# Kernel tuning notes

Hardware: AMD Instinct MI355X
Metric: run time of the kernel (lower is better)

The kernel has to match this reference:

```python
import jax, jax.numpy as jnp
import numpy as np

B, N, C, H = 32, 129, 768, 12
HID = 4 * C
EPS = 1e-5
NEG = -65504.0


def _layer_norm(x, g, b):
    mu = jnp.mean(x, axis=-1, keepdims=True)
    var = jnp.mean((x - mu) ** 2, axis=-1, keepdims=True)
    return (x - mu) / jnp.sqrt(var + EPS) * g + b


def _attn(x, m, g, b, wqkv, wproj):
    # x: [B, Nn, C], m: [B, Nn, 1] binary float mask
    Bb, Nn, Cc = x.shape
    hd = Cc // H
    xm = _layer_norm(x, g, b) * m
    qkv = (xm @ wqkv).reshape(Bb, Nn, 3, H, hd)
    q, k, v = (jnp.swapaxes(qkv[:, :, i], 1, 2) for i in range(3))  # [B,H,Nn,hd]
    att = jnp.einsum('bhqd,bhkd->bhqk', q, k) * (hd ** -0.5)
    outer = (m @ jnp.swapaxes(m, -1, -2))[:, None]  # [B,1,Nn,Nn] mask outer product
    att = jnp.where(outer == 0.0, NEG, att)
    att = jax.nn.softmax(att, axis=-1) * m[:, None]  # zero masked query rows
    out = jnp.einsum('bhqk,bhkd->bhqd', att, v)
    out = jnp.swapaxes(out, 1, 2).reshape(Bb, Nn, Cc)
    return out @ wproj


def _mlp(x, m, g, b, w1, w2):
    xm = _layer_norm(x, g, b) * m
    return jax.nn.gelu(xm @ w1, approximate=False) @ w2


def setup_inputs() -> dict:
    key = jax.random.key(0)
    ks = jax.random.split(key, 10)
    std = 0.02
    return {
        'RGB': jax.random.normal(ks[0], (B, N, C), jnp.float32),
        'NIR': jax.random.normal(ks[1], (B, N, C), jnp.float32),
        'TIR': jax.random.normal(ks[2], (B, N, C), jnp.float32),
        'mask': (jax.random.uniform(ks[3], (B, N - 1, 1)) > 0.3).astype(jnp.float32),
        'label': jax.random.randint(ks[4], (B,), 0, 171),
        # stacked params for branches [R, N, T, concat]
        'ln_g1': jnp.ones((4, C), jnp.float32),
        'ln_b1': jnp.zeros((4, C), jnp.float32),
        'w_qkv': std * jax.random.normal(ks[5], (4, C, 3 * C), jnp.float32),
        'w_proj': std * jax.random.normal(ks[6], (4, C, C), jnp.float32),
        'ln_g2': jnp.ones((4, C), jnp.float32),
        'ln_b2': jnp.zeros((4, C), jnp.float32),
        'w_fc1': std * jax.random.normal(ks[7], (4, C, HID), jnp.float32),
        'w_fc2': std * jax.random.normal(ks[8], (4, HID, C), jnp.float32),
        'out_g': jnp.ones((C,), jnp.float32),
        'out_b': jnp.zeros((C,), jnp.float32),
    }


def reference(RGB, NIR, TIR, mask, label, ln_g1, ln_b1, w_qkv, w_proj,
              ln_g2, ln_b2, w_fc1, w_fc2, out_g, out_b):
    m = jnp.concatenate([jnp.ones((RGB.shape[0], 1, 1), RGB.dtype), mask], axis=1)  # [B,N,1]

    def branch(x, i, mm):
        x = x + _attn(x, mm, ln_g1[i], ln_b1[i], w_qkv[i], w_proj[i])
        x = x + _mlp(x, mm, ln_g2[i], ln_b2[i], w_fc1[i], w_fc2[i])
        return x

    RGB = branch(RGB, 0, m)
    NIR = branch(NIR, 1, m)
    TIR = branch(TIR, 2, m)
    x = jnp.concatenate([RGB, NIR, TIR], axis=1)  # [B, 3N, C]
    m3 = jnp.tile(m, (1, 3, 1))
    x = branch(x, 3, m3)
    x = _layer_norm(x, out_g, out_b) * m3
    return x
```

## Files before the change

### kernel.cpp

```cpp
#include <hip/hip_runtime.h>

typedef unsigned short u16;
typedef __attribute__((ext_vector_type(4))) float f32x4;
typedef __attribute__((ext_vector_type(8))) short s16x8;
typedef __attribute__((ext_vector_type(4))) short s16x4;
typedef __attribute__((ext_vector_type(4))) unsigned short u16x4;

#define HH 12
#define CC 768
#define AS1(p) ((const __attribute__((address_space(1))) void*)(p))
#define AS3(p) ((__attribute__((address_space(3))) void*)(p))

__device__ inline u16 f2bf(float x){
  unsigned u = __float_as_uint(x);
  u = (u + 0x7FFFu + ((u >> 16) & 1u)) >> 16;
  return (u16)u;
}

__device__ inline f32x4 mfma32(s16x8 a, s16x8 b, f32x4 c){
  return __builtin_amdgcn_mfma_f32_16x16x32_bf16(a, b, c, 0, 0, 0);
}
__device__ inline f32x4 mfma16(s16x4 a, s16x4 b, f32x4 c){
  return __builtin_amdgcn_mfma_f32_16x16x16bf16_1k(a, b, c, 0, 0, 0);
}

__global__ void wtrans(const float* __restrict__ W, u16* __restrict__ Wt, int K, int N){
  __shared__ float tile[32][33];
  int k0 = blockIdx.x*32, n0 = blockIdx.y*32;
  const float* Wz = W + (size_t)blockIdx.z*K*N;
  u16* Wtz = Wt + (size_t)blockIdx.z*K*N;
  int tx = threadIdx.x & 31, ty = threadIdx.x >> 5;
  #pragma unroll
  for(int r = ty; r < 32; r += 8)
    tile[r][tx] = Wz[(size_t)(k0+r)*N + n0 + tx];
  __syncthreads();
  #pragma unroll
  for(int r = ty; r < 32; r += 8)
    Wtz[(size_t)(n0+r)*K + k0 + tx] = f2bf(tile[tx][r]);
}

__global__ void initcat(const float* __restrict__ R, const float* __restrict__ Nr,
                        const float* __restrict__ T, float* __restrict__ xcat){
  int idx = blockIdx.x*256 + threadIdx.x;
  const int per = 32*129*768/4;
  if(idx >= per) return;
  int z = blockIdx.y;
  const float* src = z == 0 ? R : (z == 1 ? Nr : T);
  float4 v = ((const float4*)src)[idx];
  int e = idx*4;
  int row = e / 768, c = e - row*768;
  int bb2 = row / 129, nn = row - bb2*129;
  ((float4*)xcat)[((size_t)(bb2*387 + z*129 + nn)*768 + c)/4] = v;
}

__device__ inline float maskval(const float* m, int b, int n){
  return (n == 0) ? 1.0f : m[b*128 + n - 1];
}

template<int F32OUT>
__global__ __launch_bounds__(64) void ln_mask(
    const float* __restrict__ x,
    const float* __restrict__ gg, const float* __restrict__ bb, int zsG,
    const float* __restrict__ mask,
    void* __restrict__ out, size_t zsO,
    int tpb, int zoffmul)
{
  int r = blockIdx.x, z = blockIdx.y, lane = threadIdx.x;
  int bidx = r / tpb, nn = r - bidx*tpb;
  size_t cat = (size_t)bidx*387 + z*zoffmul + nn;
  const float4* xr = (const float4*)(x + cat*CC);
  float4 v[3]; float s = 0.f, sq = 0.f;
  #pragma unroll
  for(int w = 0; w < 3; ++w){
    v[w] = xr[w*64 + lane];
    s  += v[w].x + v[w].y + v[w].z + v[w].w;
    sq += v[w].x*v[w].x + v[w].y*v[w].y + v[w].z*v[w].z + v[w].w*v[w].w;
  }
  #pragma unroll
  for(int o = 32; o; o >>= 1){ s += __shfl_xor(s, o); sq += __shfl_xor(sq, o); }
  float mu = s * (1.f/768.f);
  float var = sq * (1.f/768.f) - mu*mu;
  float rstd = rsqrtf(var + 1e-5f);
  float mv = maskval(mask, bidx, nn % 129);
  const float4* g4 = (const float4*)(gg + (size_t)z*zsG);
  const float4* b4 = (const float4*)(bb + (size_t)z*zsG);
  #pragma unroll
  for(int w = 0; w < 3; ++w){
    float4 gv = g4[w*64+lane], bv = b4[w*64+lane];
    float y0 = ((v[w].x - mu)*rstd*gv.x + bv.x) * mv;
    float y1 = ((v[w].y - mu)*rstd*gv.y + bv.y) * mv;
    float y2 = ((v[w].z - mu)*rstd*gv.z + bv.z) * mv;
    float y3 = ((v[w].w - mu)*rstd*gv.w + bv.w) * mv;
    if(F32OUT){
      ((float4*)out)[cat*(CC/4) + w*64 + lane] = make_float4(y0,y1,y2,y3);
    } else {
      u16x4 p; p.x = f2bf(y0); p.y = f2bf(y1); p.z = f2bf(y2); p.w = f2bf(y3);
      ((u16x4*)((u16*)out + z*zsO + (size_t)r*CC))[w*64 + lane] = p;
    }
  }
}

template<int EPI, int TPB>
__global__ __launch_bounds__(256) void gemm_bt(
    const u16* __restrict__ A, size_t zsA,
    const u16* __restrict__ Bt, size_t zsB,
    void* __restrict__ O, size_t zsO,
    int M, int N, int K,
    int zoffmul)
{
  __shared__ u16 As[128*32];
  __shared__ u16 Bs[128*32];
  int z = blockIdx.z;
  const u16* Az = A + zsA*(size_t)z;
  const u16* Bz = Bt + zsB*(size_t)z;

  int gx = gridDim.x, gy = gridDim.y;
  int nwg = gx*gy;
  int orig = blockIdx.x + gx*blockIdx.y;
  int q = nwg >> 3, r8 = nwg & 7;
  int xcd = orig & 7, off = orig >> 3;
  int wg = (xcd < r8 ? xcd*(q+1) : r8*(q+1) + (xcd-r8)*q) + off;
  int bx = wg / gy, by = wg - bx*gy;
  int m0 = bx*128, n0 = by*128;

  int tid = threadIdx.x, wid = tid >> 6, lane = tid & 63;
  int wr = wid >> 1, wc = wid & 1;
  int lrow = lane & 15, g4 = lane >> 4, lk8 = g4*8;

  f32x4 acc[4][4] = {};

  int e0 = wid*512 + lane*8;
  int row0 = e0 >> 5, col0 = e0 & 31;

  for(int k0 = 0; k0 < K; k0 += 32){
    #pragma unroll
    for(int j = 0; j < 2; ++j){
      int row = row0 + j*64;
      int gr = m0 + row; gr = gr < M ? gr : M - 1;
      __builtin_amdgcn_global_load_lds(AS1(Az + (size_t)gr*K + k0 + col0),
                                       AS3(As + j*2048 + wid*512), 16, 0, 0);
      __builtin_amdgcn_global_load_lds(AS1(Bz + (size_t)(n0 + row)*K + k0 + col0),
                                       AS3(Bs + j*2048 + wid*512), 16, 0, 0);
    }
    __syncthreads();
    s16x8 aF[4], bF[4];
    #pragma unroll
    for(int i = 0; i < 4; ++i){
      aF[i] = *(const s16x8*)&As[(wr*64 + i*16 + lrow)*32 + lk8];
      bF[i] = *(const s16x8*)&Bs[(wc*64 + i*16 + lrow)*32 + lk8];
    }
    #pragma unroll
    for(int i = 0; i < 4; ++i)
      #pragma unroll
      for(int jn = 0; jn < 4; ++jn)
        acc[i][jn] = mfma32(aF[i], bF[jn], acc[i][jn]);
    __syncthreads();
  }

  u16* Oz = (u16*)O + zsO*(size_t)z;
  int zb = z*zoffmul;
  #pragma unroll
  for(int i = 0; i < 4; ++i){
    #pragma unroll
    for(int r = 0; r < 4; ++r){
      int row = m0 + wr*64 + i*16 + g4*4 + r;
      if(row >= M) continue;
      #pragma unroll
      for(int jn = 0; jn < 4; ++jn){
        int col = n0 + wc*64 + jn*16 + lrow;
        float v = acc[i][jn][r];
        if constexpr (EPI == 0){
          Oz[(size_t)row*N + col] = f2bf(v);
        } else if constexpr (EPI == 1){
          float u = v*(0.7978845608f + 0.0356774081f*v*v);
          float t = 1.f - 2.f/(__expf(2.f*u) + 1.f);
          Oz[(size_t)row*N + col] = f2bf(0.5f*v*(1.f + t));
        } else {
          int bi = row / TPB, nnn = row - bi*TPB;
          size_t cat = (size_t)bi*387 + zb + nnn;
          float* dst = (float*)O + cat*CC + col;
          *dst += v;
        }
      }
    }
  }
}

template<int N_>
__global__ __launch_bounds__(256) void attn3(
    const u16* __restrict__ qkv, size_t zsQ,
    u16* __restrict__ out, size_t zsO,
    const float* __restrict__ mask)
{
  constexpr int NC  = (N_ + 63)/64;
  constexpr int NKC = NC*64;
  constexpr float SCL = 0.125f*1.44269504088896f;
  __shared__ u16 Ks[2][64][66];
  __shared__ u16 Vt[2][64][68];
  __shared__ float Msk[NKC];

  int z = blockIdx.z;
  int bh = blockIdx.y, b = bh / HH, hh = bh - b*HH;
  int tid = threadIdx.x, wid = tid >> 6, lane = tid & 63;
  int lq = lane & 15, g = lane >> 4;
  const u16* qz = qkv + zsQ*(size_t)z;
  const size_t rowbase = (size_t)b*N_;
  const u16* kbase = qz + rowbase*2304 + 768 + hh*64;
  const u16* vbase = kbase + 768;

  for(int k = tid; k < NKC; k += 256){
    float mk = 0.f;
    if(k < N_){ int nn = (N_ > 129) ? (k % 129) : k; mk = (nn == 0) ? 1.f : mask[b*128 + nn - 1]; }
    Msk[k] = (mk != 0.f) ? 0.f : -1e30f;
  }

  int q0 = blockIdx.x*64 + wid*16;
  int qrow = q0 + lq;
  int qrc = qrow < N_ ? qrow : N_ - 1;
  const u16* qptr = qz + (rowbase + qrc)*2304 + hh*64;
  s16x8 qF0 = *(const s16x8*)(qptr + g*8);
  s16x8 qF1 = *(const s16x8*)(qptr + 32 + g*8);

  int r0 = tid >> 3, c16 = tid & 7;
  s16x8 kr[2], vr[2];
  const s16x8 zv = {0,0,0,0,0,0,0,0};

  #pragma unroll
  for(int i = 0; i < 2; ++i){
    int row = r0 + i*32;
    kr[i] = (row < N_) ? *(const s16x8*)(kbase + (size_t)row*2304 + c16*8) : zv;
    vr[i] = (row < N_) ? *(const s16x8*)(vbase + (size_t)row*2304 + c16*8) : zv;
  }
  #pragma unroll
  for(int i = 0; i < 2; ++i){
    *(s16x8*)&Ks[0][r0 + i*32][c16*8] = kr[i];
    #pragma unroll
    for(int j = 0; j < 8; ++j) Vt[0][c16*8 + j][r0 + i*32] = (u16)vr[i][j];
  }
  __syncthreads();

  f32x4 o[4] = {};
  float l = 0.f;

  for(int ch = 0; ch < NC; ++ch){
    int cur = ch & 1;
    if(ch + 1 < NC){
      #pragma unroll
      for(int i = 0; i < 2; ++i){
        int row = (ch + 1)*64 + r0 + i*32;
        kr[i] = (row < N_) ? *(const s16x8*)(kbase + (size_t)row*2304 + c16*8) : zv;
        vr[i] = (row < N_) ? *(const s16x8*)(vbase + (size_t)row*2304 + c16*8) : zv;
      }
    }
    float pT[4][4];
    #pragma unroll
    for(int t = 0; t < 4; ++t){
      s16x8 kF0 = *(const s16x8*)&Ks[cur][t*16 + lq][g*8];
      s16x8 kF1 = *(const s16x8*)&Ks[cur][t*16 + lq][32 + g*8];
      f32x4 s = {0.f,0.f,0.f,0.f};
      s = mfma32(kF0, qF0, s);
      s = mfma32(kF1, qF1, s);
      const float* mrow = &Msk[ch*64 + t*16 + g*4];
      #pragma unroll
      for(int r = 0; r < 4; ++r){
        float p = exp2f(fmaf(s[r], SCL, mrow[r]));
        pT[t][r] = p;
        l += p;
      }
    }
    #pragma unroll
    for(int t = 0; t < 4; ++t){
      s16x4 pa;
      #pragma unroll
      for(int r = 0; r < 4; ++r) pa[r] = (short)f2bf(pT[t][r]);
      #pragma unroll
      for(int db = 0; db < 4; ++db){
        s16x4 vf = *(const s16x4*)&Vt[cur][db*16 + lq][t*16 + g*4];
        o[db] = mfma16(pa, vf, o[db]);
      }
    }
    if(ch + 1 < NC){
      int nxt = (ch + 1) & 1;
      #pragma unroll
      for(int i = 0; i < 2; ++i){
        *(s16x8*)&Ks[nxt][r0 + i*32][c16*8] = kr[i];
        #pragma unroll
        for(int j = 0; j < 8; ++j) Vt[nxt][c16*8 + j][r0 + i*32] = (u16)vr[i][j];
      }
      __syncthreads();
    }
  }

  l += __shfl_xor(l, 16);
  l += __shfl_xor(l, 32);
  float mq = 0.f;
  if(qrow < N_) mq = (Msk[qrow] == 0.f) ? 1.f : 0.f;
  float sc = mq / l;
  float scr[4];
  #pragma unroll
  for(int r = 0; r < 4; ++r) scr[r] = __shfl(sc, g*4 + r);

  #pragma unroll
  for(int db = 0; db < 4; ++db){
    #pragma unroll
    for(int r = 0; r < 4; ++r){
      int qq = q0 + g*4 + r;
      if(qq < N_)
        out[zsO*(size_t)z + (rowbase + qq)*CC + hh*64 + db*16 + lq] = f2bf(o[db][r]*scr[r]);
    }
  }
}

extern "C" void kernel_launch(void* const* d_in, const int* in_sizes, int n_in,
                              void* d_out, int out_size, void* d_ws, size_t ws_size,
                              hipStream_t stream)
{
  const float* RGB   = (const float*)d_in[0];
  const float* NIR   = (const float*)d_in[1];
  const float* TIR   = (const float*)d_in[2];
  const float* mask  = (const float*)d_in[3];
  const float* ln_g1 = (const float*)d_in[5];
  const float* ln_b1 = (const float*)d_in[6];
  const float* w_qkv = (const float*)d_in[7];
  const float* w_proj= (const float*)d_in[8];
  const float* ln_g2 = (const float*)d_in[9];
  const float* ln_b2 = (const float*)d_in[10];
  const float* w_fc1 = (const float*)d_in[11];
  const float* w_fc2 = (const float*)d_in[12];
  const float* out_g = (const float*)d_in[13];
  const float* out_b = (const float*)d_in[14];

  char* p = (char*)d_ws;
  u16* wqkv_t  = (u16*)p; p += (size_t)4*2304*768*2;
  u16* wproj_t = (u16*)p; p += (size_t)4*768*768*2;
  u16* w1_t    = (u16*)p; p += (size_t)4*768*3072*2;
  u16* w2_t    = (u16*)p; p += (size_t)4*3072*768*2;
  float* xcat  = (float*)p; p += (size_t)12384*768*4;
  u16* xm      = (u16*)p; p += (size_t)3*4224*768*2;
  u16* qkv     = (u16*)p; p += (size_t)3*4224*3072*2;
  u16* hbuf    = qkv;
  if((size_t)(p - (char*)d_ws) > ws_size) return;

  wtrans<<<dim3(24, 72, 4), 256, 0, stream>>>(w_qkv, wqkv_t, 768, 2304);
  wtrans<<<dim3(24, 24, 4), 256, 0, stream>>>(w_proj, wproj_t, 768, 768);
  wtrans<<<dim3(24, 96, 4), 256, 0, stream>>>(w_fc1, w1_t, 768, 3072);
  wtrans<<<dim3(96, 24, 4), 256, 0, stream>>>(w_fc2, w2_t, 3072, 768);
  initcat<<<dim3(3096, 3), 256, 0, stream>>>(RGB, NIR, TIR, xcat);

  const int M3 = 4128;
  const size_t zxm = (size_t)4224*768, zqkv = (size_t)4224*2304, zh = (size_t)4224*3072;
  ln_mask<0><<<dim3(M3,3), 64, 0, stream>>>(xcat, ln_g1, ln_b1, 768, mask, xm, zxm, 129, 129);
  gemm_bt<0,1><<<dim3(33,18,3), 256, 0, stream>>>(xm, zxm, wqkv_t, (size_t)2304*768, qkv, zqkv, M3, 2304, 768, 0);
  attn3<129><<<dim3(3,384,3), 256, 0, stream>>>(qkv, zqkv, xm, zxm, mask);
  gemm_bt<2,129><<<dim3(33,6,3), 256, 0, stream>>>(xm, zxm, wproj_t, (size_t)768*768, xcat, 0, M3, 768, 768, 129);
  ln_mask<0><<<dim3(M3,3), 64, 0, stream>>>(xcat, ln_g2, ln_b2, 768, mask, xm, zxm, 129, 129);
  gemm_bt<1,1><<<dim3(33,24,3), 256, 0, stream>>>(xm, zxm, w1_t, (size_t)768*3072, hbuf, zh, M3, 3072, 768, 0);
  gemm_bt<2,129><<<dim3(33,6,3), 256, 0, stream>>>(hbuf, zh, w2_t, (size_t)768*3072, xcat, 0, M3, 768, 3072, 129);
  const int M1 = 12384;
  ln_mask<0><<<dim3(M1,1), 64, 0, stream>>>(xcat, ln_g1 + 3*768, ln_b1 + 3*768, 0, mask, xm, 0, 387, 0);
  gemm_bt<0,1><<<dim3(97,18,1), 256, 0, stream>>>(xm, 0, wqkv_t + (size_t)3*2304*768, 0, qkv, 0, M1, 2304, 768, 0);
  attn3<387><<<dim3(7,384,1), 256, 0, stream>>>(qkv, 0, xm, 0, mask);
  gemm_bt<2,387><<<dim3(97,6,1), 256, 0, stream>>>(xm, 0, wproj_t + (size_t)3*768*768, 0, xcat, 0, M1, 768, 768, 0);
  ln_mask<0><<<dim3(M1,1), 64, 0, stream>>>(xcat, ln_g2 + 3*768, ln_b2 + 3*768, 0, mask, xm, 0, 387, 0);
  gemm_bt<1,1><<<dim3(97,24,1), 256, 0, stream>>>(xm, 0, w1_t + (size_t)3*768*3072, 0, hbuf, 0, M1, 3072, 768, 0);
  gemm_bt<2,387><<<dim3(97,6,1), 256, 0, stream>>>(hbuf, 0, w2_t + (size_t)3*768*3072, 0, xcat, 0, M1, 768, 3072, 0);
  ln_mask<1><<<dim3(M1,1), 64, 0, stream>>>(xcat, out_g, out_b, 0, mask, d_out, 0, 387, 0);
}
```

Before: 877.3 us.

## Double-buffer LDS tiles in GEMM to overlap global loads with MFMA

The GEMM kernel now keeps two LDS buffers for the A and B tiles. It issues the global-to-LDS loads for the next K-slice before computing on the current one, which removes one barrier per iteration and hides load latency behind MFMA work. Global pointers are precomputed and incremented instead of recomputing addresses each step. LDS usage doubles to 32KB per block, which may reduce occupancy. Correctness relies on a single sync per iteration covering both the read of the current buffer and the completion of the async loads.

Result: faster. 810.8 us (-7.6%).

```diff
diff --git a/kernel.cpp b/kernel.cpp
--- a/kernel.cpp
+++ b/kernel.cpp
@@ -108,8 +108,8 @@
     int M, int N, int K,
     int zoffmul)
 {
-  __shared__ u16 As[128*32];
-  __shared__ u16 Bs[128*32];
+  __shared__ u16 As[2][4096];
+  __shared__ u16 Bs[2][4096];
   int z = blockIdx.z;
   const u16* Az = A + zsA*(size_t)z;
   const u16* Bz = Bt + zsB*(size_t)z;
@@ -127,27 +127,41 @@
   int wr = wid >> 1, wc = wid & 1;
   int lrow = lane & 15, g4 = lane >> 4, lk8 = g4*8;
 
-  f32x4 acc[4][4] = {};
-
   int e0 = wid*512 + lane*8;
   int row0 = e0 >> 5, col0 = e0 & 31;
-
-  for(int k0 = 0; k0 < K; k0 += 32){
-    #pragma unroll
-    for(int j = 0; j < 2; ++j){
-      int row = row0 + j*64;
-      int gr = m0 + row; gr = gr < M ? gr : M - 1;
-      __builtin_amdgcn_global_load_lds(AS1(Az + (size_t)gr*K + k0 + col0),
-                                       AS3(As + j*2048 + wid*512), 16, 0, 0);
-      __builtin_amdgcn_global_load_lds(AS1(Bz + (size_t)(n0 + row)*K + k0 + col0),
-                                       AS3(Bs + j*2048 + wid*512), 16, 0, 0);
-    }
-    __syncthreads();
+  int ra0 = m0 + row0;      ra0 = ra0 < M ? ra0 : M - 1;
+  int ra1 = m0 + row0 + 64; ra1 = ra1 < M ? ra1 : M - 1;
+  const u16* pa0 = Az + (size_t)ra0*K + col0;
+  const u16* pa1 = Az + (size_t)ra1*K + col0;
+  const u16* pb0 = Bz + (size_t)(n0 + row0)*K + col0;
+  const u16* pb1 = Bz + (size_t)(n0 + row0 + 64)*K + col0;
+  int lofs = wid*512;
+
+  __builtin_amdgcn_global_load_lds(AS1(pa0), AS3(&As[0][lofs]),        16, 0, 0);
+  __builtin_amdgcn_global_load_lds(AS1(pa1), AS3(&As[0][lofs + 2048]), 16, 0, 0);
+  __builtin_amdgcn_global_load_lds(AS1(pb0), AS3(&Bs[0][lofs]),        16, 0, 0);
+  __builtin_amdgcn_global_load_lds(AS1(pb1), AS3(&Bs[0][lofs + 2048]), 16, 0, 0);
+  pa0 += 32; pa1 += 32; pb0 += 32; pb1 += 32;
+  __syncthreads();
+
+  f32x4 acc[4][4] = {};
+  int NT = K >> 5;
+  int cur = 0;
+
+  for(int t = 0; t < NT; ++t){
+    if(t + 1 < NT){
+      int nxt = cur ^ 1;
+      __builtin_amdgcn_global_load_lds(AS1(pa0), AS3(&As[nxt][lofs]),        16, 0, 0);
+      __builtin_amdgcn_global_load_lds(AS1(pa1), AS3(&As[nxt][lofs + 2048]), 16, 0, 0);
+      __builtin_amdgcn_global_load_lds(AS1(pb0), AS3(&Bs[nxt][lofs]),        16, 0, 0);
+      __builtin_amdgcn_global_load_lds(AS1(pb1), AS3(&Bs[nxt][lofs + 2048]), 16, 0, 0);
+      pa0 += 32; pa1 += 32; pb0 += 32; pb1 += 32;
+    }
     s16x8 aF[4], bF[4];
     #pragma unroll
     for(int i = 0; i < 4; ++i){
-      aF[i] = *(const s16x8*)&As[(wr*64 + i*16 + lrow)*32 + lk8];
-      bF[i] = *(const s16x8*)&Bs[(wc*64 + i*16 + lrow)*32 + lk8];
+      aF[i] = *(const s16x8*)&As[cur][(wr*64 + i*16 + lrow)*32 + lk8];
+      bF[i] = *(const s16x8*)&Bs[cur][(wc*64 + i*16 + lrow)*32 + lk8];
     }
     #pragma unroll
     for(int i = 0; i < 4; ++i)
@@ -155,6 +169,7 @@
       for(int jn = 0; jn < 4; ++jn)
         acc[i][jn] = mfma32(aF[i], bF[jn], acc[i][jn]);
     __syncthreads();
+    cur ^= 1;
   }
 
   u16* Oz = (u16*)O + zsO*(size_t)z;
```

## Double-buffer GEMM LDS tiles with BK=64, XOR swizzle, and async prefetch

Applied to the files above, without the earlier changes.

Reworks the bf16 GEMM main loop to use two LDS buffers with a K-tile of 64. The next tile is prefetched via global_load_lds while the current one is consumed, and an explicit vmcnt wait replaces the full sync. Columns are XOR-swizzled by row to reduce LDS bank conflicts on fragment reads. LDS use grows to 64KB per block, which may reduce occupancy, and the loop assumes K is a multiple of 64.

After: 850.6 us. 1.03x faster.

```diff
diff --git a/kernel.cpp b/kernel.cpp
--- a/kernel.cpp
+++ b/kernel.cpp
@@ -108,8 +108,8 @@
     int M, int N, int K,
     int zoffmul)
 {
-  __shared__ u16 As[128*32];
-  __shared__ u16 Bs[128*32];
+  __shared__ u16 As[2][128*64];
+  __shared__ u16 Bs[2][128*64];
   int z = blockIdx.z;
   const u16* Az = A + zsA*(size_t)z;
   const u16* Bz = Bt + zsB*(size_t)z;
@@ -125,36 +125,64 @@
 
   int tid = threadIdx.x, wid = tid >> 6, lane = tid & 63;
   int wr = wid >> 1, wc = wid & 1;
-  int lrow = lane & 15, g4 = lane >> 4, lk8 = g4*8;
+  int lrow = lane & 15, g4 = lane >> 4;
+
+  int srow = tid >> 3;
+  int swcol = ((tid & 7) ^ (srow & 7)) * 8;
+  const u16 *pa[4], *pb[4];
+  #pragma unroll
+  for(int i = 0; i < 4; ++i){
+    int ra = m0 + srow + i*32; ra = ra < M ? ra : M - 1;
+    pa[i] = Az + (size_t)ra*K + swcol;
+    pb[i] = Bz + (size_t)(n0 + srow + i*32)*K + swcol;
+  }
+  int dofs = tid*8;
+
+  auto stage = [&](int b){
+    #pragma unroll
+    for(int i = 0; i < 4; ++i)
+      __builtin_amdgcn_global_load_lds(AS1(pa[i]), AS3(&As[b][dofs + i*2048]), 16, 0, 0);
+    #pragma unroll
+    for(int i = 0; i < 4; ++i)
+      __builtin_amdgcn_global_load_lds(AS1(pb[i]), AS3(&Bs[b][dofs + i*2048]), 16, 0, 0);
+    #pragma unroll
+    for(int i = 0; i < 4; ++i){ pa[i] += 64; pb[i] += 64; }
+  };
+
+  int xs0 = ((0*4 + g4) ^ (lrow & 7)) * 8;
+  int xs1 = ((1*4 + g4) ^ (lrow & 7)) * 8;
+
+  int NT = K >> 6;
+  stage(0);
 
   f32x4 acc[4][4] = {};
-
-  int e0 = wid*512 + lane*8;
-  int row0 = e0 >> 5, col0 = e0 & 31;
-
-  for(int k0 = 0; k0 < K; k0 += 32){
-    #pragma unroll
-    for(int j = 0; j < 2; ++j){
-      int row = row0 + j*64;
-      int gr = m0 + row; gr = gr < M ? gr : M - 1;
-      __builtin_amdgcn_global_load_lds(AS1(Az + (size_t)gr*K + k0 + col0),
-                                       AS3(As + j*2048 + wid*512), 16, 0, 0);
-      __builtin_amdgcn_global_load_lds(AS1(Bz + (size_t)(n0 + row)*K + k0 + col0),
-                                       AS3(Bs + j*2048 + wid*512), 16, 0, 0);
-    }
-    __syncthreads();
-    s16x8 aF[4], bF[4];
-    #pragma unroll
-    for(int i = 0; i < 4; ++i){
-      aF[i] = *(const s16x8*)&As[(wr*64 + i*16 + lrow)*32 + lk8];
-      bF[i] = *(const s16x8*)&Bs[(wc*64 + i*16 + lrow)*32 + lk8];
-    }
-    #pragma unroll
-    for(int i = 0; i < 4; ++i)
-      #pragma unroll
-      for(int jn = 0; jn < 4; ++jn)
-        acc[i][jn] = mfma32(aF[i], bF[jn], acc[i][jn]);
-    __syncthreads();
+  int cur = 0;
+
+  for(int t = 0; t < NT; ++t){
+    if(t + 1 < NT){
+      stage(cur ^ 1);
+      asm volatile("s_waitcnt vmcnt(8)" ::: "memory");
+    } else {
+      asm volatile("s_waitcnt vmcnt(0)" ::: "memory");
+    }
+    __builtin_amdgcn_s_barrier();
+    #pragma unroll
+    for(int kk = 0; kk < 2; ++kk){
+      int xs = kk ? xs1 : xs0;
+      s16x8 aF[4], bF[4];
+      #pragma unroll
+      for(int i = 0; i < 4; ++i){
+        aF[i] = *(const s16x8*)&As[cur][(wr*64 + i*16 + lrow)*64 + xs];
+        bF[i] = *(const s16x8*)&Bs[cur][(wc*64 + i*16 + lrow)*64 + xs];
+      }
+      #pragma unroll
+      for(int i = 0; i < 4; ++i)
+        #pragma unroll
+        for(int jn = 0; jn < 4; ++jn)
+          acc[i][jn] = mfma32(aF[i], bF[jn], acc[i][jn]);
+    }
+    __builtin_amdgcn_s_barrier();
+    cur ^= 1;
   }
 
   u16* Oz = (u16*)O + zsO*(size_t)z;
```
